# Kernel optimization log

Hardware: AMD Instinct MI355X
Metric: run time of the kernel (lower is better)

Reference implementation:

```python
import jax, jax.numpy as jnp
import numpy as np

EMBED_DIM_LIST = [256, 512]
NUM_HEADS_LIST = [4, 8]
MAX_EMBED = 512
N_BASE = 8                       # = max(num_heads_list)
MAX_HS = max(EMBED_DIM_LIST) // min(NUM_HEADS_LIST)  # 128


def _config_masks():
    # One {0,1} mask per (emb, heads) config, shape [n_cfg, N_BASE, MAX_HS, MAX_EMBED].
    # Mask encodes: slice base weight [:head_size, :emb], zero-pad to (MAX_HS, MAX_EMBED),
    # and that only the first `heads` base heads receive a contribution.
    r = np.arange(MAX_HS)[:, None]
    c = np.arange(MAX_EMBED)[None, :]
    masks = []
    for emb in EMBED_DIM_LIST:
        for heads in NUM_HEADS_LIST:
            hs = emb // heads
            m2 = ((r < hs) & (c < emb)).astype(np.float32)      # [MAX_HS, MAX_EMBED]
            hm = (np.arange(N_BASE) < heads).astype(np.float32)  # [N_BASE]
            masks.append(hm[:, None, None] * m2[None])
    return jnp.asarray(np.stack(masks))  # [4, 8, 128, 512]

_CFG_MASKS = _config_masks()


def setup_inputs() -> dict:
    key = jax.random.key(0)
    k0, k1, k2, k3, k4 = jax.random.split(key, 5)
    B, T = 4, 2048
    x = jax.random.normal(k0, (B, T, MAX_EMBED), dtype=jnp.float32)
    weights = jax.random.uniform(k1, (len(EMBED_DIM_LIST) * len(NUM_HEADS_LIST),), dtype=jnp.float32)
    s = 0.02
    base_K = jax.random.normal(k2, (N_BASE, MAX_HS, MAX_EMBED), dtype=jnp.float32) * s
    base_Q = jax.random.normal(k3, (N_BASE, MAX_HS, MAX_EMBED), dtype=jnp.float32) * s
    base_V = jax.random.normal(k4, (N_BASE, MAX_HS, MAX_EMBED), dtype=jnp.float32) * s
    return {"x": x, "weights": weights, "base_K": base_K, "base_Q": base_Q, "base_V": base_V}


def reference(x, weights, base_K, base_Q, base_V):
    B, T, C = x.shape
    # Weight mixing: sum_i weights[i] * (padded slice of base weight) for each base head.
    eff = jnp.einsum('i,ihde->hde', weights, _CFG_MASKS)  # [H, MAX_HS, MAX_EMBED]
    Wk = eff * base_K
    Wq = eff * base_Q
    Wv = eff * base_V
    # Projections for all base heads at once: F.linear(x, W) == x @ W.T
    k = jnp.einsum('btc,hdc->bhtd', x, Wk)
    q = jnp.einsum('btc,hdc->bhtd', x, Wq)
    v = jnp.einsum('btc,hdc->bhtd', x, Wv)
    # Causal self-attention; scale uses k.shape[-1] == MAX_HS (padded head size), as in source.
    scale = 1.0 / jnp.sqrt(jnp.asarray(MAX_HS, dtype=x.dtype))
    att = jnp.einsum('bhtd,bhsd->bhts', q, k) * scale       # [B, H, T, T]
    tril = jnp.tril(jnp.ones((T, T), dtype=bool))
    att = jnp.where(tril, att, -jnp.inf)
    wei = jax.nn.softmax(att, axis=-1)                       # dropout = identity (eval)
    out = jnp.einsum('bhts,bhsd->bhtd', wei, v)              # [B, H, T, MAX_HS]
    # torch.cat(head_out_list, dim=-1) in head order == transpose + reshape
    return out.transpose(0, 2, 1, 3).reshape(B, T, N_BASE * MAX_HS)
```

## Files before the change

kernel.cpp:

```cpp
#include <hip/hip_runtime.h>
#include <hip/hip_bf16.h>
#include <stdint.h>

typedef __attribute__((ext_vector_type(8))) short bf16x8;
typedef __attribute__((ext_vector_type(4))) float f32x4;
typedef __attribute__((ext_vector_type(16))) float f32x16;

#define MFMA16(a,b,c) __builtin_amdgcn_mfma_f32_16x16x32_bf16((a),(b),(c),0,0,0)
#define MFMA32(a,b,c) __builtin_amdgcn_mfma_f32_32x32x16_bf16((a),(b),(c),0,0,0)
#define AS1 __attribute__((address_space(1)))
#define AS3 __attribute__((address_space(3)))

__device__ inline short f2bf(float f) {
    union { __hip_bfloat16 h; short s; } u;
    u.h = __float2bfloat16(f);
    return u.s;
}
__device__ inline uint32_t pack_bf16(float a, float b) {
    union { __hip_bfloat16 h; uint16_t u; } ua, ub;
    ua.h = __float2bfloat16(a); ub.h = __float2bfloat16(b);
    return (uint32_t)ua.u | ((uint32_t)ub.u << 16);
}

#if __has_builtin(__builtin_amdgcn_permlane32_swap)
#define SWAP32(x, y, a, b) { auto _r = __builtin_amdgcn_permlane32_swap((a),(b),false,false); \
                             (x) = _r[0]; (y) = _r[1]; }
#else
#define SWAP32(x, y, a, b) { uint32_t _ta = __shfl_xor((uint32_t)(a),32); \
                             uint32_t _tb = __shfl_xor((uint32_t)(b),32); \
                             (x) = hh_ ? _tb : (a); (y) = hh_ ? (b) : _ta; }
#endif

#define QSCALE 0.12751879523879295f

#define NW (8*128*512)
#define NX4 (8192*512/4)

__global__ void prep_kernel(const float* __restrict__ x,
                            const float* __restrict__ w,
                            const float* __restrict__ bK,
                            const float* __restrict__ bQ,
                            const float* __restrict__ bV,
                            short* __restrict__ xb,
                            short* __restrict__ W)
{
    const float w0 = w[0], w1 = w[1], w2 = w[2], w3 = w[3];
    for (int i = blockIdx.x * blockDim.x + threadIdx.x; i < NW + NX4;
         i += gridDim.x * blockDim.x) {
        if (i < NW) {
            int e = i & 511;
            int d = (i >> 9) & 127;
            int h = i >> 16;
            float eff = 0.f;
            if (h < 4) { eff += w2; if (d < 64 && e < 256) eff += w0; }
            if (d < 32 && e < 256) eff += w1;
            if (d < 64) eff += w3;
            W[i]          = f2bf(eff * bK[i]);
            W[i + NW]     = f2bf(eff * bQ[i] * QSCALE);
            W[i + 2*NW]   = f2bf(eff * bV[i]);
        } else {
            int j = i - NW;
            float4 v = ((const float4*)x)[j];
            short4 o;
            o.x = f2bf(v.x); o.y = f2bf(v.y); o.z = f2bf(v.z); o.w = f2bf(v.w);
            ((short4*)xb)[j] = o;
        }
    }
}

__global__ __launch_bounds__(256)
void proj_gemm(const short* __restrict__ A,
               const short* __restrict__ Bw,
               short* __restrict__ qkv)
{
    __shared__ short S[128 * 128];
    short* As = S;
    short* Bs = S + 128 * 64;
    const int tid = threadIdx.x;
    const int lane = tid & 63;
    const int wave = tid >> 6;
    const int wr = wave >> 1, wc = wave & 1;
    const int l15 = lane & 15, lk = lane >> 4;

    const int wg = (blockIdx.x & 7) * 192 + (blockIdx.x >> 3);
    const int bm = (wg / 24) * 128;
    const int bn = (wg % 24) * 128;

    char* Ab = (char*)As;
    char* Bb = (char*)Bs;
    char* Sb = (char*)S;
    f32x4 acc[4][4] = {};

    for (int k0 = 0; k0 < 512; k0 += 64) {
        __syncthreads();
#pragma unroll
        for (int i = 0; i < 4; ++i) {
            int c = i * 256 + tid;
            int lin = c * 16;
            int row = lin >> 7;
            int cof = ((lin & 127) ^ ((row & 7) << 4)) >> 1;
            __builtin_amdgcn_global_load_lds(
                (const AS1 void*)(A + (size_t)(bm + row) * 512 + k0 + cof),
                (AS3 void*)(As + c * 8), 16, 0, 0);
            __builtin_amdgcn_global_load_lds(
                (const AS1 void*)(Bw + (size_t)(bn + row) * 512 + k0 + cof),
                (AS3 void*)(Bs + c * 8), 16, 0, 0);
        }
        __syncthreads();
#pragma unroll
        for (int kk = 0; kk < 2; ++kk) {
            bf16x8 af[4], bfv[4];
#pragma unroll
            for (int mi = 0; mi < 4; ++mi) {
                int row = wr * 64 + mi * 16 + l15;
                af[mi] = *(const bf16x8*)(Ab + ((row * 128 + kk * 64 + lk * 16) ^ ((row & 7) << 4)));
            }
#pragma unroll
            for (int ni = 0; ni < 4; ++ni) {
                int row = wc * 64 + ni * 16 + l15;
                bfv[ni] = *(const bf16x8*)(Bb + ((row * 128 + kk * 64 + lk * 16) ^ ((row & 7) << 4)));
            }
#pragma unroll
            for (int mi = 0; mi < 4; ++mi)
#pragma unroll
                for (int ni = 0; ni < 4; ++ni)
                    acc[mi][ni] = MFMA16(af[mi], bfv[ni], acc[mi][ni]);
        }
    }

    const int proj = bn >> 10;
    const int b = bm >> 11;
    const int bh = b * 8 + ((bn & 1023) >> 7);
    const int tbase = bm & 2047;

    __syncthreads();
    if (proj == 2) {
#pragma unroll
        for (int mi = 0; mi < 4; ++mi) {
#pragma unroll
            for (int ni = 0; ni < 4; ++ni) {
                int dl = wc * 64 + ni * 16 + l15;
                int tlb = wr * 64 + mi * 16 + lk * 4;
                int byte0 = (dl * 256 + tlb * 2) ^ ((dl & 7) << 4);
                *(uint32_t*)(Sb + byte0)     = pack_bf16(acc[mi][ni][0], acc[mi][ni][1]);
                *(uint32_t*)(Sb + byte0 + 4) = pack_bf16(acc[mi][ni][2], acc[mi][ni][3]);
            }
        }
    } else {
#pragma unroll
        for (int mi = 0; mi < 4; ++mi) {
#pragma unroll
            for (int ni = 0; ni < 4; ++ni) {
                int dl = wc * 64 + ni * 16 + l15;
#pragma unroll
                for (int r = 0; r < 4; ++r) {
                    int tl = wr * 64 + mi * 16 + lk * 4 + r;
                    *(short*)(Sb + ((tl * 256 + dl * 2) ^ ((tl & 7) << 4))) = f2bf(acc[mi][ni][r]);
                }
            }
        }
    }
    __syncthreads();

    short* dst;
    if (proj == 2)
        dst = qkv + (size_t)2 * (32 * 2048 * 128) + (size_t)bh * 128 * 2048;
    else
        dst = qkv + (size_t)proj * (32 * 2048 * 128) + (size_t)bh * 2048 * 128;

#pragma unroll
    for (int i = 0; i < 8; ++i) {
        int c = i * 256 + tid;
        int row = c >> 4;
        uint4 v = *(const uint4*)(Sb + row * 256 + (((c & 15) * 16) ^ ((row & 7) << 4)));
        if (proj == 2) {
            *(uint4*)(dst + (size_t)row * 2048 + tbase + (c & 15) * 8) = v;
        } else {
            *(uint4*)(dst + (size_t)(tbase + row) * 128 + (c & 15) * 8) = v;
        }
    }
}

__device__ inline void stage64(const short* __restrict__ Kp,
                               const short* __restrict__ Vp,
                               int j0, char* smem, int buf)
{
    short* kls = (short*)(smem + (buf << 15));
    short* vls = kls + 8192;
    const int tid = threadIdx.x;
#pragma unroll
    for (int i = 0; i < 2; ++i) {
        int c = i * 512 + tid;
        int slot = c >> 6, t = c & 63;
        __builtin_amdgcn_global_load_lds(
            (const AS1 void*)(Kp + (size_t)(j0 + t) * 128 + slot * 8),
            (AS3 void*)(kls + c * 8), 16, 0, 0);
    }
#pragma unroll
    for (int i = 0; i < 2; ++i) {
        int c = i * 512 + tid;
        int slot = c >> 7, d = c & 127;
        __builtin_amdgcn_global_load_lds(
            (const AS1 void*)(Vp + (size_t)d * 2048 + j0 + slot * 8),
            (AS3 void*)(vls + c * 8), 16, 0, 0);
    }
}

__global__ __launch_bounds__(512, 2)
void attn_kernel(const short* __restrict__ qkv, float* __restrict__ out)
{
    extern __shared__ char smem[];
    const int tid = threadIdx.x, lane = tid & 63, wave = tid >> 6;
    const int l31 = lane & 31;
    const int hh_ = lane >> 5;

    const int bh = blockIdx.x & 31;
    const int a = blockIdx.x >> 5;

    const int qc = wave & 3;
    const int kvh = wave >> 2;

    const size_t HSTRIDE = (size_t)2048 * 128;
    const short* Kp = qkv + (size_t)bh * HSTRIDE;
    const short* Qp = qkv + (size_t)32 * HSTRIDE + (size_t)bh * HSTRIDE;
    const short* Vp = qkv + (size_t)64 * HSTRIDE + (size_t)bh * HSTRIDE;

    for (int sidx = 0; sidx < 2; ++sidx) {
        const int sp = sidx ? (15 - a) : a;
        const int q0 = sp * 128;
        const int nt = 2 * sp + 2;
        const int qwave = q0 + qc * 32;
        const int qglob = qwave + l31;

        __syncthreads();

        bf16x8 qf[8];
        {
            const short* qrow = Qp + (size_t)(q0 + qc * 32 + l31) * 128 + hh_ * 8;
#pragma unroll
            for (int dblk = 0; dblk < 8; ++dblk)
                qf[dblk] = *(const bf16x8*)(qrow + dblk * 16);
        }

        float mrow = -1e30f, lrow = 0.f;
        f32x16 acco[4] = {};

        stage64(Kp, Vp, 0, smem, 0);

        for (int jt = 0; jt < nt; ++jt) {
            const int j0 = jt << 6;
            __builtin_amdgcn_s_barrier();
            if (jt + 1 < nt) {
                stage64(Kp, Vp, (jt + 1) << 6, smem, (jt + 1) & 1);
                asm volatile("s_waitcnt vmcnt(4)" ::: "memory");
            } else {
                asm volatile("s_waitcnt vmcnt(0)" ::: "memory");
            }
            __builtin_amdgcn_sched_barrier(0);
            __builtin_amdgcn_s_barrier();
            __builtin_amdgcn_sched_barrier(0);

            const int kv0 = j0 + kvh * 32;
            if (kv0 <= qwave + 31) {
                const short* kls = (const short*)(smem + ((jt & 1) << 15));
                const short* vls = kls + 8192;

                f32x16 sacc = {};
                __builtin_amdgcn_s_setprio(1);
#pragma unroll
                for (int dblk = 0; dblk < 8; ++dblk) {
                    bf16x8 kf = *(const bf16x8*)(kls + ((dblk * 2 + hh_) * 64 + kvh * 32 + l31) * 8);
                    sacc = MFMA32(kf, qf[dblk], sacc);
                }
                __builtin_amdgcn_s_setprio(0);

                if (kv0 + 31 > qwave) {
#pragma unroll
                    for (int r = 0; r < 16; ++r) {
                        int kvglob = kv0 + (r & 3) + 8 * (r >> 2) + 4 * hh_;
                        if (kvglob > qglob) sacc[r] = -1e30f;
                    }
                }

                float pmax = -1e30f;
#pragma unroll
                for (int r = 0; r < 16; r += 4) {
                    float a2 = fmaxf(sacc[r], sacc[r + 1]);
                    float b2 = fmaxf(sacc[r + 2], sacc[r + 3]);
                    pmax = fmaxf(pmax, fmaxf(a2, b2));
                }
                pmax = fmaxf(pmax, __shfl_xor(pmax, 32));

                if (!__all(pmax - mrow <= 11.5416f)) {
                    float mn = fmaxf(mrow, pmax);
                    float alpha = __builtin_amdgcn_exp2f(mrow - mn);
                    mrow = mn;
                    lrow *= alpha;
#pragma unroll
                    for (int r = 0; r < 16; ++r) {
                        float ar = __shfl(alpha, (r & 3) + 8 * (r >> 2) + 4 * hh_);
#pragma unroll
                        for (int dt = 0; dt < 4; ++dt) acco[dt][r] *= ar;
                    }
                }

                float psum = 0.f;
                uint32_t pkA[4], pkB[4];
#pragma unroll
                for (int sg = 0; sg < 4; ++sg) {
                    float p0 = __builtin_amdgcn_exp2f(sacc[4 * sg + 0] - mrow);
                    float p1 = __builtin_amdgcn_exp2f(sacc[4 * sg + 1] - mrow);
                    float p2 = __builtin_amdgcn_exp2f(sacc[4 * sg + 2] - mrow);
                    float p3 = __builtin_amdgcn_exp2f(sacc[4 * sg + 3] - mrow);
                    psum += (p0 + p1) + (p2 + p3);
                    pkA[sg] = pack_bf16(p0, p1);
                    pkB[sg] = pack_bf16(p2, p3);
                }
                psum += __shfl_xor(psum, 32);
                lrow += psum;

                __builtin_amdgcn_s_setprio(1);
#pragma unroll
                for (int kb = 0; kb < 2; ++kb) {
                    uint32_t r0, r1, r2, r3;
                    SWAP32(r0, r2, pkA[2 * kb], pkA[2 * kb + 1]);
                    SWAP32(r1, r3, pkB[2 * kb], pkB[2 * kb + 1]);
                    union { uint32_t u[4]; bf16x8 v; } pa;
                    pa.u[0] = r0; pa.u[1] = r1; pa.u[2] = r2; pa.u[3] = r3;
                    const int slot = kvh * 4 + kb * 2 + hh_;
#pragma unroll
                    for (int dt = 0; dt < 4; ++dt) {
                        bf16x8 vf = *(const bf16x8*)(vls + (slot * 128 + dt * 32 + l31) * 8);
                        acco[dt] = MFMA32(pa.v, vf, acco[dt]);
                    }
                }
                __builtin_amdgcn_s_setprio(0);
            }
        }

        __syncthreads();
        float* ex = (float*)smem;
        float* ml = (float*)(smem + 65536);
        if (kvh == 1) {
            float* dst = ex + qc * 4096;
#pragma unroll
            for (int dt = 0; dt < 4; ++dt)
#pragma unroll
                for (int r = 0; r < 16; ++r)
                    dst[(dt * 16 + r) * 64 + lane] = acco[dt][r];
            ml[qc * 128 + lane * 2 + 0] = mrow;
            ml[qc * 128 + lane * 2 + 1] = lrow;
        }
        __syncthreads();
        if (kvh == 0) {
            float m1 = ml[qc * 128 + lane * 2 + 0];
            float l1 = ml[qc * 128 + lane * 2 + 1];
            float M  = fmaxf(mrow, m1);
            float av = __builtin_amdgcn_exp2f(mrow - M);
            float bv = __builtin_amdgcn_exp2f(m1 - M);
            float lf = lrow * av + l1 * bv;
            float sA = av / lf, sB = bv / lf;
            const float* src = ex + qc * 4096;
            const int bb = bh >> 3, hd = bh & 7;
#pragma unroll
            for (int r = 0; r < 16; ++r) {
                int ql = (r & 3) + 8 * (r >> 2) + 4 * hh_;
                float sa = __shfl(sA, ql);
                float sb = __shfl(sB, ql);
                int t = qwave + ql;
                float* o = out + (size_t)(bb * 2048 + t) * 1024 + hd * 128 + l31;
#pragma unroll
                for (int dt = 0; dt < 4; ++dt)
                    o[dt * 32] = acco[dt][r] * sa + src[(dt * 16 + r) * 64 + lane] * sb;
            }
        }
    }
}

extern "C" void kernel_launch(void* const* d_in, const int* in_sizes, int n_in,
                              void* d_out, int out_size, void* d_ws, size_t ws_size,
                              hipStream_t stream) {
    const float* x  = (const float*)d_in[0];
    const float* w  = (const float*)d_in[1];
    const float* bK = (const float*)d_in[2];
    const float* bQ = (const float*)d_in[3];
    const float* bV = (const float*)d_in[4];

    short* xb  = (short*)d_ws;
    short* W   = (short*)((char*)d_ws + 8388608);
    short* qkv = (short*)((char*)d_ws + 8388608 + 3145728);
    float* out = (float*)d_out;

    hipFuncSetAttribute((const void*)attn_kernel,
                        hipFuncAttributeMaxDynamicSharedMemorySize, 67584);

    prep_kernel<<<2048, 256, 0, stream>>>(x, w, bK, bQ, bV, xb, W);
    proj_gemm<<<64 * 24, 256, 0, stream>>>(xb, W, qkv);
    attn_kernel<<<256, 512, 67584, stream>>>(qkv, out);
}
```

Measured before the change: 110.6 us.

## Deepen KV staging to four LDS buffers with XOR-swizzled K/V layout

Replaces the double-buffered K/V staging in the attention kernel with a 4-deep ring that prefetches three tiles ahead and uses one barrier per iteration instead of two. K and V tiles are stored in LDS in a row-major XOR-swizzled layout instead of slot-major, and the read addresses are adjusted to match, to cut bank conflicts. This raises dynamic LDS from about 66 KB to 128 KB per block, which may limit blocks per CU (launch bounds ask for 2). The epilogue reuses the smem buffer, so leftover in-flight loads are a risk; a final vmcnt(0) wait is added.

```diff
diff --git a/kernel.cpp b/kernel.cpp
--- a/kernel.cpp
+++ b/kernel.cpp
@@ -191,17 +191,18 @@
 #pragma unroll
     for (int i = 0; i < 2; ++i) {
         int c = i * 512 + tid;
-        int slot = c >> 6, t = c & 63;
+        int lin = c * 16;
+        int rk = lin >> 8;
+        int kof = ((lin & 255) ^ ((rk & 15) << 4)) >> 1;
         __builtin_amdgcn_global_load_lds(
-            (const AS1 void*)(Kp + (size_t)(j0 + t) * 128 + slot * 8),
+            (const AS1 void*)(Kp + (size_t)(j0 + rk) * 128 + kof),
             (AS3 void*)(kls + c * 8), 16, 0, 0);
-    }
-#pragma unroll
-    for (int i = 0; i < 2; ++i) {
-        int c = i * 512 + tid;
-        int slot = c >> 7, d = c & 127;
+        int rv = lin >> 8;
+        int p = (lin & 255) ^ ((rv & 15) << 4);
+        int d = rv * 2 + (p >> 7);
+        int t = (p & 127) >> 1;
         __builtin_amdgcn_global_load_lds(
-            (const AS1 void*)(Vp + (size_t)d * 2048 + j0 + slot * 8),
+            (const AS1 void*)(Vp + (size_t)d * 2048 + j0 + t),
             (AS3 void*)(vls + c * 8), 16, 0, 0);
     }
 }
@@ -246,30 +247,30 @@
         f32x16 acco[4] = {};
 
         stage64(Kp, Vp, 0, smem, 0);
+        if (nt > 1) stage64(Kp, Vp, 64, smem, 1);
+        if (nt > 2) stage64(Kp, Vp, 128, smem, 2);
+        if (nt > 2)      { asm volatile("s_waitcnt vmcnt(8)" ::: "memory"); }
+        else             { asm volatile("s_waitcnt vmcnt(4)" ::: "memory"); }
+        __builtin_amdgcn_sched_barrier(0);
+        __builtin_amdgcn_s_barrier();
+        __builtin_amdgcn_sched_barrier(0);
 
         for (int jt = 0; jt < nt; ++jt) {
             const int j0 = jt << 6;
-            __builtin_amdgcn_s_barrier();
-            if (jt + 1 < nt) {
-                stage64(Kp, Vp, (jt + 1) << 6, smem, (jt + 1) & 1);
-                asm volatile("s_waitcnt vmcnt(4)" ::: "memory");
-            } else {
-                asm volatile("s_waitcnt vmcnt(0)" ::: "memory");
-            }
-            __builtin_amdgcn_sched_barrier(0);
-            __builtin_amdgcn_s_barrier();
-            __builtin_amdgcn_sched_barrier(0);
+            if (jt + 3 < nt)
+                stage64(Kp, Vp, (jt + 3) << 6, smem, (jt + 3) & 3);
 
             const int kv0 = j0 + kvh * 32;
             if (kv0 <= qwave + 31) {
-                const short* kls = (const short*)(smem + ((jt & 1) << 15));
-                const short* vls = kls + 8192;
+                const char* Kb = smem + ((size_t)(jt & 3) << 15);
+                const char* Vb = Kb + 16384;
 
                 f32x16 sacc = {};
+                const int krow = kvh * 32 + l31;
                 __builtin_amdgcn_s_setprio(1);
 #pragma unroll
                 for (int dblk = 0; dblk < 8; ++dblk) {
-                    bf16x8 kf = *(const bf16x8*)(kls + ((dblk * 2 + hh_) * 64 + kvh * 32 + l31) * 8);
+                    bf16x8 kf = *(const bf16x8*)(Kb + ((krow * 256 + dblk * 32 + hh_ * 16) ^ ((krow & 15) << 4)));
                     sacc = MFMA32(kf, qf[dblk], sacc);
                 }
                 __builtin_amdgcn_s_setprio(0);
@@ -327,14 +328,26 @@
                     SWAP32(r1, r3, pkB[2 * kb], pkB[2 * kb + 1]);
                     union { uint32_t u[4]; bf16x8 v; } pa;
                     pa.u[0] = r0; pa.u[1] = r1; pa.u[2] = r2; pa.u[3] = r3;
-                    const int slot = kvh * 4 + kb * 2 + hh_;
+                    const int slot = kvh * 2 + kb;
 #pragma unroll
                     for (int dt = 0; dt < 4; ++dt) {
-                        bf16x8 vf = *(const bf16x8*)(vls + (slot * 128 + dt * 32 + l31) * 8);
+                        int d = dt * 32 + l31;
+                        int r = d >> 1;
+                        int inner = ((d & 1) << 7) + slot * 32 + hh_ * 16;
+                        bf16x8 vf = *(const bf16x8*)(Vb + (r * 256 + (inner ^ ((r & 15) << 4))));
                         acco[dt] = MFMA32(pa.v, vf, acco[dt]);
                     }
                 }
                 __builtin_amdgcn_s_setprio(0);
+            }
+
+            if (jt + 1 < nt) {
+                if (jt + 4 <= nt)      { asm volatile("s_waitcnt vmcnt(8)" ::: "memory"); }
+                else if (jt + 3 == nt) { asm volatile("s_waitcnt vmcnt(4)" ::: "memory"); }
+                else                   { asm volatile("s_waitcnt vmcnt(0)" ::: "memory"); }
+                __builtin_amdgcn_sched_barrier(0);
+                __builtin_amdgcn_s_barrier();
+                __builtin_amdgcn_sched_barrier(0);
             }
         }
 
@@ -374,6 +387,7 @@
                     o[dt * 32] = acco[dt][r] * sa + src[(dt * 16 + r) * 64 + lane] * sb;
             }
         }
+        asm volatile("s_waitcnt vmcnt(0)" ::: "memory");
     }
 }
 
@@ -392,9 +406,9 @@
     float* out = (float*)d_out;
 
     hipFuncSetAttribute((const void*)attn_kernel,
-                        hipFuncAttributeMaxDynamicSharedMemorySize, 67584);
+                        hipFuncAttributeMaxDynamicSharedMemorySize, 131072);
 
     prep_kernel<<<2048, 256, 0, stream>>>(x, w, bK, bQ, bV, xb, W);
     proj_gemm<<<64 * 24, 256, 0, stream>>>(xb, W, qkv);
-    attn_kernel<<<256, 512, 67584, stream>>>(qkv, out);
-}
+    attn_kernel<<<256, 512, 131072, stream>>>(qkv, out);
+}
```

Measured after the change: 107.9 us. -2.5%, faster.

## Enlarge attention KV tile to 128 with swizzled LDS layout and single barrier

Applied to the files above, without the earlier changes.

The attention kernel now stages 128 KV rows per iteration instead of 64, with each wave handling two 32-row sub-tiles. K and V staging goes into an XOR-swizzled LDS layout whose offsets are precomputed once per thread, and the loop uses one barrier per tile instead of two. The goal is to halve the loop iterations and barrier/softmax bookkeeping and to reduce LDS bank conflicts. In exchange LDS use doubles to 128 KB, which can limit how many blocks fit per CU, and the larger diagonal tiles do more masked, wasted work.

```diff
diff --git a/kernel.cpp b/kernel.cpp
--- a/kernel.cpp
+++ b/kernel.cpp
@@ -181,31 +181,6 @@
     }
 }
 
-__device__ inline void stage64(const short* __restrict__ Kp,
-                               const short* __restrict__ Vp,
-                               int j0, char* smem, int buf)
-{
-    short* kls = (short*)(smem + (buf << 15));
-    short* vls = kls + 8192;
-    const int tid = threadIdx.x;
-#pragma unroll
-    for (int i = 0; i < 2; ++i) {
-        int c = i * 512 + tid;
-        int slot = c >> 6, t = c & 63;
-        __builtin_amdgcn_global_load_lds(
-            (const AS1 void*)(Kp + (size_t)(j0 + t) * 128 + slot * 8),
-            (AS3 void*)(kls + c * 8), 16, 0, 0);
-    }
-#pragma unroll
-    for (int i = 0; i < 2; ++i) {
-        int c = i * 512 + tid;
-        int slot = c >> 7, d = c & 127;
-        __builtin_amdgcn_global_load_lds(
-            (const AS1 void*)(Vp + (size_t)d * 2048 + j0 + slot * 8),
-            (AS3 void*)(vls + c * 8), 16, 0, 0);
-    }
-}
-
 __global__ __launch_bounds__(512, 2)
 void attn_kernel(const short* __restrict__ qkv, float* __restrict__ out)
 {
@@ -225,10 +200,39 @@
     const short* Qp = qkv + (size_t)32 * HSTRIDE + (size_t)bh * HSTRIDE;
     const short* Vp = qkv + (size_t)64 * HSTRIDE + (size_t)bh * HSTRIDE;
 
+    int koffs[4], voffs[4];
+#pragma unroll
+    for (int i = 0; i < 4; ++i) {
+        int c = i * 512 + tid;
+        int rk = c >> 4;
+        int kof = (((c * 16) & 255) ^ ((rk & 15) << 4)) >> 1;
+        koffs[i] = rk * 128 + kof;
+        int sub = c >> 10, cc = c & 1023;
+        int rv = cc >> 4;
+        int p = ((cc * 16) & 255) ^ ((rv & 15) << 4);
+        int d = 2 * rv + (p >> 7);
+        int t = (p & 127) >> 1;
+        voffs[i] = d * 2048 + sub * 64 + t;
+    }
+
+#define STAGE128(J0, BUF) {                                                   \
+        char* _b = smem + ((BUF) << 16);                                      \
+        _Pragma("unroll")                                                     \
+        for (int i = 0; i < 4; ++i) {                                         \
+            int c = i * 512 + tid;                                            \
+            __builtin_amdgcn_global_load_lds(                                 \
+                (const AS1 void*)(Kp + koffs[i] + (J0) * 128),                \
+                (AS3 void*)(_b + c * 16), 16, 0, 0);                          \
+            __builtin_amdgcn_global_load_lds(                                 \
+                (const AS1 void*)(Vp + voffs[i] + (J0)),                      \
+                (AS3 void*)(_b + 32768 + c * 16), 16, 0, 0);                  \
+        }                                                                     \
+    }
+
     for (int sidx = 0; sidx < 2; ++sidx) {
         const int sp = sidx ? (15 - a) : a;
         const int q0 = sp * 128;
-        const int nt = 2 * sp + 2;
+        const int nt = sp + 1;
         const int qwave = q0 + qc * 32;
         const int qglob = qwave + l31;
 
@@ -245,50 +249,55 @@
         float mrow = -1e30f, lrow = 0.f;
         f32x16 acco[4] = {};
 
-        stage64(Kp, Vp, 0, smem, 0);
+        STAGE128(0, 0);
+        asm volatile("s_waitcnt vmcnt(0)" ::: "memory");
+        __builtin_amdgcn_sched_barrier(0);
+        __builtin_amdgcn_s_barrier();
+        __builtin_amdgcn_sched_barrier(0);
 
         for (int jt = 0; jt < nt; ++jt) {
-            const int j0 = jt << 6;
-            __builtin_amdgcn_s_barrier();
-            if (jt + 1 < nt) {
-                stage64(Kp, Vp, (jt + 1) << 6, smem, (jt + 1) & 1);
-                asm volatile("s_waitcnt vmcnt(4)" ::: "memory");
-            } else {
-                asm volatile("s_waitcnt vmcnt(0)" ::: "memory");
-            }
-            __builtin_amdgcn_sched_barrier(0);
-            __builtin_amdgcn_s_barrier();
-            __builtin_amdgcn_sched_barrier(0);
-
-            const int kv0 = j0 + kvh * 32;
+            const int j0 = jt << 7;
+            if (jt + 1 < nt)
+                STAGE128((jt + 1) << 7, (jt + 1) & 1);
+
+            const int kv0 = j0 + kvh * 64;
             if (kv0 <= qwave + 31) {
-                const short* kls = (const short*)(smem + ((jt & 1) << 15));
-                const short* vls = kls + 8192;
-
-                f32x16 sacc = {};
+                const char* Kb = smem + ((jt & 1) << 16);
+                const char* Vb = Kb + 32768 + (kvh << 14);
+
+                f32x16 sacc[2] = {};
                 __builtin_amdgcn_s_setprio(1);
 #pragma unroll
                 for (int dblk = 0; dblk < 8; ++dblk) {
-                    bf16x8 kf = *(const bf16x8*)(kls + ((dblk * 2 + hh_) * 64 + kvh * 32 + l31) * 8);
-                    sacc = MFMA32(kf, qf[dblk], sacc);
+#pragma unroll
+                    for (int kvt = 0; kvt < 2; ++kvt) {
+                        int krow = kvh * 64 + kvt * 32 + l31;
+                        bf16x8 kf = *(const bf16x8*)(Kb + krow * 256 +
+                            ((dblk * 32 + hh_ * 16) ^ ((krow & 15) << 4)));
+                        sacc[kvt] = MFMA32(kf, qf[dblk], sacc[kvt]);
+                    }
                 }
                 __builtin_amdgcn_s_setprio(0);
 
-                if (kv0 + 31 > qwave) {
-#pragma unroll
-                    for (int r = 0; r < 16; ++r) {
-                        int kvglob = kv0 + (r & 3) + 8 * (r >> 2) + 4 * hh_;
-                        if (kvglob > qglob) sacc[r] = -1e30f;
+                if (kv0 + 63 > qwave) {
+#pragma unroll
+                    for (int kvt = 0; kvt < 2; ++kvt)
+#pragma unroll
+                        for (int r = 0; r < 16; ++r) {
+                            int kvglob = kv0 + kvt * 32 + (r & 3) + 8 * (r >> 2) + 4 * hh_;
+                            if (kvglob > qglob) sacc[kvt][r] = -1e30f;
+                        }
+                }
+
+                float pmax = -1e30f;
+#pragma unroll
+                for (int kvt = 0; kvt < 2; ++kvt)
+#pragma unroll
+                    for (int r = 0; r < 16; r += 4) {
+                        float a2 = fmaxf(sacc[kvt][r], sacc[kvt][r + 1]);
+                        float b2 = fmaxf(sacc[kvt][r + 2], sacc[kvt][r + 3]);
+                        pmax = fmaxf(pmax, fmaxf(a2, b2));
                     }
-                }
-
-                float pmax = -1e30f;
-#pragma unroll
-                for (int r = 0; r < 16; r += 4) {
-                    float a2 = fmaxf(sacc[r], sacc[r + 1]);
-                    float b2 = fmaxf(sacc[r + 2], sacc[r + 3]);
-                    pmax = fmaxf(pmax, fmaxf(a2, b2));
-                }
                 pmax = fmaxf(pmax, __shfl_xor(pmax, 32));
 
                 if (!__all(pmax - mrow <= 11.5416f)) {
@@ -305,36 +314,48 @@
                 }
 
                 float psum = 0.f;
-                uint32_t pkA[4], pkB[4];
-#pragma unroll
-                for (int sg = 0; sg < 4; ++sg) {
-                    float p0 = __builtin_amdgcn_exp2f(sacc[4 * sg + 0] - mrow);
-                    float p1 = __builtin_amdgcn_exp2f(sacc[4 * sg + 1] - mrow);
-                    float p2 = __builtin_amdgcn_exp2f(sacc[4 * sg + 2] - mrow);
-                    float p3 = __builtin_amdgcn_exp2f(sacc[4 * sg + 3] - mrow);
-                    psum += (p0 + p1) + (p2 + p3);
-                    pkA[sg] = pack_bf16(p0, p1);
-                    pkB[sg] = pack_bf16(p2, p3);
-                }
+                uint32_t pkA[2][4], pkB[2][4];
+#pragma unroll
+                for (int kvt = 0; kvt < 2; ++kvt)
+#pragma unroll
+                    for (int sg = 0; sg < 4; ++sg) {
+                        float p0 = __builtin_amdgcn_exp2f(sacc[kvt][4 * sg + 0] - mrow);
+                        float p1 = __builtin_amdgcn_exp2f(sacc[kvt][4 * sg + 1] - mrow);
+                        float p2 = __builtin_amdgcn_exp2f(sacc[kvt][4 * sg + 2] - mrow);
+                        float p3 = __builtin_amdgcn_exp2f(sacc[kvt][4 * sg + 3] - mrow);
+                        psum += (p0 + p1) + (p2 + p3);
+                        pkA[kvt][sg] = pack_bf16(p0, p1);
+                        pkB[kvt][sg] = pack_bf16(p2, p3);
+                    }
                 psum += __shfl_xor(psum, 32);
                 lrow += psum;
 
                 __builtin_amdgcn_s_setprio(1);
 #pragma unroll
-                for (int kb = 0; kb < 2; ++kb) {
+                for (int w = 0; w < 4; ++w) {
+                    const int kvt = w >> 1, kbl = w & 1;
                     uint32_t r0, r1, r2, r3;
-                    SWAP32(r0, r2, pkA[2 * kb], pkA[2 * kb + 1]);
-                    SWAP32(r1, r3, pkB[2 * kb], pkB[2 * kb + 1]);
+                    SWAP32(r0, r2, pkA[kvt][2 * kbl], pkA[kvt][2 * kbl + 1]);
+                    SWAP32(r1, r3, pkB[kvt][2 * kbl], pkB[kvt][2 * kbl + 1]);
                     union { uint32_t u[4]; bf16x8 v; } pa;
                     pa.u[0] = r0; pa.u[1] = r1; pa.u[2] = r2; pa.u[3] = r3;
-                    const int slot = kvh * 4 + kb * 2 + hh_;
 #pragma unroll
                     for (int dt = 0; dt < 4; ++dt) {
-                        bf16x8 vf = *(const bf16x8*)(vls + (slot * 128 + dt * 32 + l31) * 8);
+                        int d = dt * 32 + l31;
+                        int r = d >> 1;
+                        int inner = ((d & 1) << 7) + w * 32 + hh_ * 16;
+                        bf16x8 vf = *(const bf16x8*)(Vb + r * 256 + (inner ^ ((r & 15) << 4)));
                         acco[dt] = MFMA32(pa.v, vf, acco[dt]);
                     }
                 }
                 __builtin_amdgcn_s_setprio(0);
+            }
+
+            if (jt + 1 < nt) {
+                asm volatile("s_waitcnt vmcnt(0)" ::: "memory");
+                __builtin_amdgcn_sched_barrier(0);
+                __builtin_amdgcn_s_barrier();
+                __builtin_amdgcn_sched_barrier(0);
             }
         }
 
@@ -374,7 +395,9 @@
                     o[dt * 32] = acco[dt][r] * sa + src[(dt * 16 + r) * 64 + lane] * sb;
             }
         }
-    }
+        asm volatile("s_waitcnt vmcnt(0)" ::: "memory");
+    }
+#undef STAGE128
 }
 
 extern "C" void kernel_launch(void* const* d_in, const int* in_sizes, int n_in,
@@ -392,9 +415,9 @@
     float* out = (float*)d_out;
 
     hipFuncSetAttribute((const void*)attn_kernel,
-                        hipFuncAttributeMaxDynamicSharedMemorySize, 67584);
+                        hipFuncAttributeMaxDynamicSharedMemorySize, 131072);
 
     prep_kernel<<<2048, 256, 0, stream>>>(x, w, bK, bQ, bV, xb, W);
     proj_gemm<<<64 * 24, 256, 0, stream>>>(xb, W, qkv);
-    attn_kernel<<<256, 512, 67584, stream>>>(qkv, out);
-}
+    attn_kernel<<<256, 512, 131072, stream>>>(qkv, out);
+}
```

Measured after the change: 100.0 us. 9.6% less time.

## Widen attention blocks to 16 waves with 128-key tiles and LDS-resident Q

Applied to the files above, without the earlier changes.

The attention kernel moves to 1024-thread blocks: four query chunks times four key sub-tiles of 32, over 128-key tiles instead of 64. Q now lives in swizzled LDS rather than registers. K and V are staged with an XOR swizzle into double-buffered 64 KB slots. The merge becomes a two-level tree reduction of the four partial softmax states. This halves the number of loop iterations and barriers per tile and frees registers. In exchange it needs 160 KB of LDS (one block per CU), waits vmcnt(0) at every iteration's end, which weakens prefetch overlap, and adds extra barriers in the reduction.

```diff
diff --git a/kernel.cpp b/kernel.cpp
--- a/kernel.cpp
+++ b/kernel.cpp
@@ -181,32 +181,52 @@
     }
 }
 
-__device__ inline void stage64(const short* __restrict__ Kp,
-                               const short* __restrict__ Vp,
-                               int j0, char* smem, int buf)
+__device__ inline void stage_kv(const short* __restrict__ Kp,
+                                const short* __restrict__ Vp,
+                                int j0, char* smem, int buf)
 {
-    short* kls = (short*)(smem + (buf << 15));
-    short* vls = kls + 8192;
+    short* kls = (short*)(smem + (buf << 16));
+    short* vls = kls + 16384;
     const int tid = threadIdx.x;
 #pragma unroll
     for (int i = 0; i < 2; ++i) {
-        int c = i * 512 + tid;
-        int slot = c >> 6, t = c & 63;
+        int c = i * 1024 + tid;
+        int rk = c >> 4;
+        int kof = (((c * 16) & 255) ^ ((rk & 15) << 4)) >> 1;
         __builtin_amdgcn_global_load_lds(
-            (const AS1 void*)(Kp + (size_t)(j0 + t) * 128 + slot * 8),
+            (const AS1 void*)(Kp + (size_t)(j0 + rk) * 128 + kof),
             (AS3 void*)(kls + c * 8), 16, 0, 0);
     }
 #pragma unroll
     for (int i = 0; i < 2; ++i) {
-        int c = i * 512 + tid;
-        int slot = c >> 7, d = c & 127;
+        int c = i * 1024 + tid;
+        int sub = c >> 10, cc = c & 1023;
+        int rv = cc >> 4;
+        int p = ((cc * 16) & 255) ^ ((rv & 15) << 4);
+        int d = 2 * rv + (p >> 7);
+        int t = (p & 127) >> 1;
         __builtin_amdgcn_global_load_lds(
-            (const AS1 void*)(Vp + (size_t)d * 2048 + j0 + slot * 8),
+            (const AS1 void*)(Vp + (size_t)d * 2048 + j0 + sub * 64 + t),
             (AS3 void*)(vls + c * 8), 16, 0, 0);
     }
 }
 
-__global__ __launch_bounds__(512, 2)
+__device__ inline void stage_q(const short* __restrict__ Qp, int q0, char* smem)
+{
+    short* qls = (short*)(smem + 131072);
+    const int tid = threadIdx.x;
+#pragma unroll
+    for (int i = 0; i < 2; ++i) {
+        int c = i * 1024 + tid;
+        int rk = c >> 4;
+        int kof = (((c * 16) & 255) ^ ((rk & 15) << 4)) >> 1;
+        __builtin_amdgcn_global_load_lds(
+            (const AS1 void*)(Qp + (size_t)(q0 + rk) * 128 + kof),
+            (AS3 void*)(qls + c * 8), 16, 0, 0);
+    }
+}
+
+__global__ __launch_bounds__(1024, 4)
 void attn_kernel(const short* __restrict__ qkv, float* __restrict__ out)
 {
     extern __shared__ char smem[];
@@ -218,59 +238,60 @@
     const int a = blockIdx.x >> 5;
 
     const int qc = wave & 3;
-    const int kvh = wave >> 2;
+    const int kvq = wave >> 2;
 
     const size_t HSTRIDE = (size_t)2048 * 128;
     const short* Kp = qkv + (size_t)bh * HSTRIDE;
     const short* Qp = qkv + (size_t)32 * HSTRIDE + (size_t)bh * HSTRIDE;
     const short* Vp = qkv + (size_t)64 * HSTRIDE + (size_t)bh * HSTRIDE;
 
+    const int hh16 = hh_ * 16;
+    const int krow = kvq * 32 + l31;
+    const int kbase = krow * 256, kswz = (krow & 15) << 4;
+    const int qrow = qc * 32 + l31;
+    const int qbase = qrow * 256, qswz = (qrow & 15) << 4;
+    const int dlow = (l31 & 1) << 7;
+    const int rb0 = (l31 >> 1) * 256;
+    const int vswz = ((l31 >> 1) & 15) << 4;
+
     for (int sidx = 0; sidx < 2; ++sidx) {
         const int sp = sidx ? (15 - a) : a;
         const int q0 = sp * 128;
-        const int nt = 2 * sp + 2;
+        const int nt = sp + 1;
         const int qwave = q0 + qc * 32;
         const int qglob = qwave + l31;
 
         __syncthreads();
 
-        bf16x8 qf[8];
-        {
-            const short* qrow = Qp + (size_t)(q0 + qc * 32 + l31) * 128 + hh_ * 8;
-#pragma unroll
-            for (int dblk = 0; dblk < 8; ++dblk)
-                qf[dblk] = *(const bf16x8*)(qrow + dblk * 16);
-        }
+        stage_q(Qp, q0, smem);
+        stage_kv(Kp, Vp, 0, smem, 0);
 
         float mrow = -1e30f, lrow = 0.f;
         f32x16 acco[4] = {};
 
-        stage64(Kp, Vp, 0, smem, 0);
+        asm volatile("s_waitcnt vmcnt(0)" ::: "memory");
+        __builtin_amdgcn_sched_barrier(0);
+        __builtin_amdgcn_s_barrier();
+        __builtin_amdgcn_sched_barrier(0);
 
         for (int jt = 0; jt < nt; ++jt) {
-            const int j0 = jt << 6;
-            __builtin_amdgcn_s_barrier();
-            if (jt + 1 < nt) {
-                stage64(Kp, Vp, (jt + 1) << 6, smem, (jt + 1) & 1);
-                asm volatile("s_waitcnt vmcnt(4)" ::: "memory");
-            } else {
-                asm volatile("s_waitcnt vmcnt(0)" ::: "memory");
-            }
-            __builtin_amdgcn_sched_barrier(0);
-            __builtin_amdgcn_s_barrier();
-            __builtin_amdgcn_sched_barrier(0);
-
-            const int kv0 = j0 + kvh * 32;
+            const int j0 = jt << 7;
+            if (jt + 1 < nt)
+                stage_kv(Kp, Vp, (jt + 1) << 7, smem, (jt + 1) & 1);
+
+            const int kv0 = j0 + kvq * 32;
             if (kv0 <= qwave + 31) {
-                const short* kls = (const short*)(smem + ((jt & 1) << 15));
-                const short* vls = kls + 8192;
+                const char* Kb = smem + ((jt & 1) << 16);
+                const char* Vb = Kb + 32768 + ((kvq >> 1) << 14);
+                const char* Qb = smem + 131072;
 
                 f32x16 sacc = {};
                 __builtin_amdgcn_s_setprio(1);
 #pragma unroll
                 for (int dblk = 0; dblk < 8; ++dblk) {
-                    bf16x8 kf = *(const bf16x8*)(kls + ((dblk * 2 + hh_) * 64 + kvh * 32 + l31) * 8);
-                    sacc = MFMA32(kf, qf[dblk], sacc);
+                    bf16x8 kf = *(const bf16x8*)(Kb + kbase + ((dblk * 32 + hh16) ^ kswz));
+                    bf16x8 qf = *(const bf16x8*)(Qb + qbase + ((dblk * 32 + hh16) ^ qswz));
+                    sacc = MFMA32(kf, qf, sacc);
                 }
                 __builtin_amdgcn_s_setprio(0);
 
@@ -327,34 +348,76 @@
                     SWAP32(r1, r3, pkB[2 * kb], pkB[2 * kb + 1]);
                     union { uint32_t u[4]; bf16x8 v; } pa;
                     pa.u[0] = r0; pa.u[1] = r1; pa.u[2] = r2; pa.u[3] = r3;
-                    const int slot = kvh * 4 + kb * 2 + hh_;
+                    const int w = (kvq & 1) * 2 + kb;
 #pragma unroll
                     for (int dt = 0; dt < 4; ++dt) {
-                        bf16x8 vf = *(const bf16x8*)(vls + (slot * 128 + dt * 32 + l31) * 8);
+                        bf16x8 vf = *(const bf16x8*)(Vb + rb0 + dt * 4096 +
+                                     ((dlow + w * 32 + hh16) ^ vswz));
                         acco[dt] = MFMA32(pa.v, vf, acco[dt]);
                     }
                 }
                 __builtin_amdgcn_s_setprio(0);
             }
+
+            if (jt + 1 < nt) {
+                asm volatile("s_waitcnt vmcnt(0)" ::: "memory");
+                __builtin_amdgcn_sched_barrier(0);
+                __builtin_amdgcn_s_barrier();
+                __builtin_amdgcn_sched_barrier(0);
+            }
         }
 
         __syncthreads();
         float* ex = (float*)smem;
-        float* ml = (float*)(smem + 65536);
-        if (kvh == 1) {
-            float* dst = ex + qc * 4096;
+        float* ml = (float*)(smem + 131072);
+
+        if (kvq >= 2) {
+            int rg = qc * 2 + (kvq - 2);
+            float* dst = ex + rg * 4096;
 #pragma unroll
             for (int dt = 0; dt < 4; ++dt)
 #pragma unroll
                 for (int r = 0; r < 16; ++r)
                     dst[(dt * 16 + r) * 64 + lane] = acco[dt][r];
-            ml[qc * 128 + lane * 2 + 0] = mrow;
-            ml[qc * 128 + lane * 2 + 1] = lrow;
-        }
-        __syncthreads();
-        if (kvh == 0) {
-            float m1 = ml[qc * 128 + lane * 2 + 0];
-            float l1 = ml[qc * 128 + lane * 2 + 1];
+            ml[rg * 128 + lane * 2 + 0] = mrow;
+            ml[rg * 128 + lane * 2 + 1] = lrow;
+        }
+        __syncthreads();
+        if (kvq < 2) {
+            int rg = qc * 2 + kvq;
+            float m1 = ml[rg * 128 + lane * 2 + 0];
+            float l1 = ml[rg * 128 + lane * 2 + 1];
+            float M  = fmaxf(mrow, m1);
+            float av = __builtin_amdgcn_exp2f(mrow - M);
+            float bv = __builtin_amdgcn_exp2f(m1 - M);
+            mrow = M;
+            lrow = lrow * av + l1 * bv;
+            const float* src = ex + rg * 4096;
+#pragma unroll
+            for (int r = 0; r < 16; ++r) {
+                int ql = (r & 3) + 8 * (r >> 2) + 4 * hh_;
+                float ar = __shfl(av, ql);
+                float br = __shfl(bv, ql);
+#pragma unroll
+                for (int dt = 0; dt < 4; ++dt)
+                    acco[dt][r] = acco[dt][r] * ar + src[(dt * 16 + r) * 64 + lane] * br;
+            }
+        }
+        __syncthreads();
+        if (kvq == 1) {
+            float* dst = ex + qc * 4096;
+#pragma unroll
+            for (int dt = 0; dt < 4; ++dt)
+#pragma unroll
+                for (int r = 0; r < 16; ++r)
+                    dst[(dt * 16 + r) * 64 + lane] = acco[dt][r];
+            ml[1024 + qc * 128 + lane * 2 + 0] = mrow;
+            ml[1024 + qc * 128 + lane * 2 + 1] = lrow;
+        }
+        __syncthreads();
+        if (kvq == 0) {
+            float m1 = ml[1024 + qc * 128 + lane * 2 + 0];
+            float l1 = ml[1024 + qc * 128 + lane * 2 + 1];
             float M  = fmaxf(mrow, m1);
             float av = __builtin_amdgcn_exp2f(mrow - M);
             float bv = __builtin_amdgcn_exp2f(m1 - M);
@@ -392,9 +455,9 @@
     float* out = (float*)d_out;
 
     hipFuncSetAttribute((const void*)attn_kernel,
-                        hipFuncAttributeMaxDynamicSharedMemorySize, 67584);
+                        hipFuncAttributeMaxDynamicSharedMemorySize, 163840);
 
     prep_kernel<<<2048, 256, 0, stream>>>(x, w, bK, bQ, bV, xb, W);
     proj_gemm<<<64 * 24, 256, 0, stream>>>(xb, W, qkv);
-    attn_kernel<<<256, 512, 67584, stream>>>(qkv, out);
-}
+    attn_kernel<<<256, 1024, 163840, stream>>>(qkv, out);
+}
```

After: 145.7 us. 31.7% more time.
